# Optimization experiments

Measured on AMD Instinct MI355X. Metric: run time of the kernel, lower is better.

The kernel has to match this reference:

```python
import jax, jax.numpy as jnp
import numpy as np

HEADS = 4
DIM_HEAD = 32
DIM = 128
HIDDEN = HEADS * DIM_HEAD  # 128
EPS = 1e-12  # F.normalize eps


def rms_norm(x, g):
    # F.normalize(x, dim=1) * g * sqrt(C)  with g shape [C]
    n = jnp.sqrt(jnp.sum(x * x, axis=1, keepdims=True))
    return x / jnp.maximum(n, EPS) * g[None, :, None, None] * (x.shape[1] ** 0.5)


def setup_inputs() -> dict:
    key = jax.random.key(0)
    ks = jax.random.split(key, 6)
    x = jax.random.normal(ks[0], (16, DIM, 128, 128), dtype=jnp.float32)
    g1 = jnp.ones((DIM,), dtype=jnp.float32)
    w_qkv = jax.random.normal(ks[1], (3 * HIDDEN, DIM), dtype=jnp.float32) * (1.0 / np.sqrt(DIM))
    w_out = jax.random.normal(ks[2], (DIM, HIDDEN), dtype=jnp.float32) * (1.0 / np.sqrt(HIDDEN))
    b_out = jax.random.normal(ks[3], (DIM,), dtype=jnp.float32) * 0.01
    g2 = jnp.ones((DIM,), dtype=jnp.float32)
    return {"x": x, "g1": g1, "w_qkv": w_qkv, "w_out": w_out, "b_out": b_out, "g2": g2}


def reference(x, g1, w_qkv, w_out, b_out, g2):
    B, C, H, W = x.shape
    n = H * W
    scale = DIM_HEAD ** -0.5
    xn = rms_norm(x, g1)
    # 1x1 conv (no bias) == channel matmul
    qkv = jnp.einsum('oc,bchw->bohw', w_qkv, xn)  # [B, 3*HIDDEN, H, W]
    q, k, v = jnp.split(qkv, 3, axis=1)
    # 'b (h c) x y -> b h c (x y)'
    def to_heads(t):
        return t.reshape(B, HEADS, DIM_HEAD, n)
    q, k, v = to_heads(q), to_heads(k), to_heads(v)
    q = jax.nn.softmax(q, axis=2) * scale   # softmax over head-dim d
    k = jax.nn.softmax(k, axis=3)           # softmax over tokens n
    context = jnp.einsum('bhdn,bhen->bhde', k, v)  # [B,H,d,e] small
    out = jnp.einsum('bhde,bhdn->bhen', context, q)  # [B,H,e,n]
    out = out.reshape(B, HIDDEN, H, W)
    out = jnp.einsum('oc,bchw->bohw', w_out, out) + b_out[None, :, None, None]
    return rms_norm(out, g2)
```

## Files before the change

### kernel.cpp

```cpp
#include <hip/hip_runtime.h>
#include <hip/hip_bf16.h>

#define NTOK 16384
#define SQRT_C 11.313708498984761f
#define QSCALE 0.17677669529663687f

typedef __attribute__((ext_vector_type(8))) short v8s;
typedef __attribute__((ext_vector_type(4))) float v4f;

__device__ inline short f2bf(float f) {
    __hip_bfloat16 h = __float2bfloat16(f);
    return __builtin_bit_cast(short, h);
}
__device__ inline float bf2f(short s) {
    unsigned u = ((unsigned)(unsigned short)s) << 16;
    return __builtin_bit_cast(float, u);
}

__global__ void k0_cvt(const float* __restrict__ wq, short* __restrict__ wbf) {
    int i = blockIdx.x * 256 + threadIdx.x;
    wbf[i] = f2bf(wq[i]);
}

__global__ __launch_bounds__(256, 2) void k1_qkv(
    const float* __restrict__ x, const float* __restrict__ g1,
    const short* __restrict__ wbf, short* __restrict__ qfrag,
    float* __restrict__ pS, float* __restrict__ pC)
{
    __shared__ float xbuf[128][36];
    __shared__ short xn[32][136];
    __shared__ short kvbuf[256][40];
    __shared__ short qbuf[128][33];
    __shared__ float nrm[8][32];
    __shared__ float scl[32];
    __shared__ float g1s[128];

    const int tid = threadIdx.x;
    const int lane = tid & 63;
    const int w = tid >> 6;
    const int qd = lane >> 4;
    const int lm = lane & 15;
    const int b = blockIdx.x >> 5;
    const int chunk = blockIdx.x & 31;
    const size_t xbase = (size_t)b * 128 * NTOK;

    if (tid < 128) g1s[tid] = g1[tid];

    v8s wA[6][4];
    #pragma unroll
    for (int rg = 0; rg < 6; ++rg)
        #pragma unroll
        for (int kk = 0; kk < 4; ++kk)
            wA[rg][kk] = *(const v8s*)(wbf + (96 * w + rg * 16 + lm) * 128 + kk * 32 + qd * 8);

    v4f cacc[2][2];
    #pragma unroll
    for (int i = 0; i < 2; ++i)
        #pragma unroll
        for (int j = 0; j < 2; ++j)
            cacc[i][j] = (v4f){0.f, 0.f, 0.f, 0.f};
    float accS = 0.f;

    for (int st = 0; st < 16; ++st) {
        const int t0 = chunk * 512 + st * 32;
        __syncthreads();
        #pragma unroll
        for (int p = 0; p < 4; ++p) {
            int idx = p * 256 + tid;
            int c = idx >> 3, tq = idx & 7;
            *(float4*)&xbuf[c][tq * 4] =
                *(const float4*)(x + xbase + (size_t)c * NTOK + t0 + tq * 4);
        }
        __syncthreads();
        {
            int t = tid & 31, g = tid >> 5;
            float s = 0.f;
            #pragma unroll
            for (int j = 0; j < 16; ++j) { float v = xbuf[g * 16 + j][t]; s += v * v; }
            nrm[g][t] = s;
        }
        __syncthreads();
        if (tid < 32) {
            float s = 0.f;
            #pragma unroll
            for (int g = 0; g < 8; ++g) s += nrm[g][tid];
            scl[tid] = SQRT_C / fmaxf(sqrtf(s), 1e-12f);
        }
        __syncthreads();
        {
            int t = tid & 31, g = tid >> 5;
            float sc = scl[t];
            #pragma unroll
            for (int j = 0; j < 16; ++j) {
                int c = g * 16 + j;
                xn[t][c] = f2bf(xbuf[c][t] * sc * g1s[c]);
            }
        }
        __syncthreads();
        v4f C[6][2];
        #pragma unroll
        for (int rg = 0; rg < 6; ++rg) {
            C[rg][0] = (v4f){0.f, 0.f, 0.f, 0.f};
            C[rg][1] = (v4f){0.f, 0.f, 0.f, 0.f};
        }
        #pragma unroll
        for (int kk = 0; kk < 4; ++kk) {
            v8s B0 = *(const v8s*)&xn[lm][kk * 32 + qd * 8];
            v8s B1 = *(const v8s*)&xn[16 + lm][kk * 32 + qd * 8];
            #pragma unroll
            for (int rg = 0; rg < 6; ++rg) {
                C[rg][0] = __builtin_amdgcn_mfma_f32_16x16x32_bf16(wA[rg][kk], B0, C[rg][0], 0, 0, 0);
                C[rg][1] = __builtin_amdgcn_mfma_f32_16x16x32_bf16(wA[rg][kk], B1, C[rg][1], 0, 0, 0);
            }
        }
        #pragma unroll
        for (int pr = 0; pr < 3; ++pr) {
            const int R = 96 * w + 32 * pr;
            if (R < 128) {
                #pragma unroll
                for (int tg = 0; tg < 2; ++tg) {
                    float e0[4], e1[4];
                    float m = -1e30f;
                    #pragma unroll
                    for (int r = 0; r < 4; ++r) {
                        e0[r] = C[2 * pr][tg][r];
                        e1[r] = C[2 * pr + 1][tg][r];
                        m = fmaxf(m, fmaxf(e0[r], e1[r]));
                    }
                    m = fmaxf(m, __shfl_xor(m, 16, 64));
                    m = fmaxf(m, __shfl_xor(m, 32, 64));
                    float s = 0.f;
                    #pragma unroll
                    for (int r = 0; r < 4; ++r) {
                        e0[r] = __expf(e0[r] - m);
                        e1[r] = __expf(e1[r] - m);
                        s += e0[r] + e1[r];
                    }
                    s += __shfl_xor(s, 16, 64);
                    s += __shfl_xor(s, 32, 64);
                    float inv = QSCALE / s;
                    int col = tg * 16 + lm;
                    #pragma unroll
                    for (int r = 0; r < 4; ++r) {
                        qbuf[R + qd * 4 + r][col]      = f2bf(e0[r] * inv);
                        qbuf[R + 16 + qd * 4 + r][col] = f2bf(e1[r] * inv);
                    }
                }
            } else {
                #pragma unroll
                for (int f = 0; f < 2; ++f) {
                    const int rg = 2 * pr + f;
                    const int R2 = R + 16 * f;
                    const bool isk = (R2 < 256);
                    #pragma unroll
                    for (int tg = 0; tg < 2; ++tg) {
                        int col = tg * 16 + lm;
                        #pragma unroll
                        for (int r = 0; r < 4; ++r) {
                            float val = C[rg][tg][r];
                            if (isk) val = __expf(val);
                            kvbuf[R2 - 128 + qd * 4 + r][col] = f2bf(val);
                        }
                    }
                }
            }
        }
        __syncthreads();
        if (tid < 128) {
            const short* row = &kvbuf[tid][0];
            float s = 0.f;
            #pragma unroll
            for (int j = 0; j < 32; ++j) s += bf2f(row[j]);
            accS += s;
        }
        {
            const int tb0 = t0 >> 4;
            #pragma unroll
            for (int tbl = 0; tbl < 2; ++tbl) {
                v8s pk;
                #pragma unroll
                for (int j = 0; j < 8; ++j)
                    pk[j] = qbuf[w * 32 + qd * 8 + j][tbl * 16 + lm];
                *(v8s*)(qfrag + ((((size_t)b * 1024 + tb0 + tbl) * 4 + w) << 9) + lane * 8) = pk;
            }
        }
        {
            v8s A0 = *(const v8s*)&kvbuf[w * 32 + lm][qd * 8];
            v8s A1 = *(const v8s*)&kvbuf[w * 32 + 16 + lm][qd * 8];
            v8s B0 = *(const v8s*)&kvbuf[128 + w * 32 + lm][qd * 8];
            v8s B1 = *(const v8s*)&kvbuf[128 + w * 32 + 16 + lm][qd * 8];
            cacc[0][0] = __builtin_amdgcn_mfma_f32_16x16x32_bf16(A0, B0, cacc[0][0], 0, 0, 0);
            cacc[0][1] = __builtin_amdgcn_mfma_f32_16x16x32_bf16(A0, B1, cacc[0][1], 0, 0, 0);
            cacc[1][0] = __builtin_amdgcn_mfma_f32_16x16x32_bf16(A1, B0, cacc[1][0], 0, 0, 0);
            cacc[1][1] = __builtin_amdgcn_mfma_f32_16x16x32_bf16(A1, B1, cacc[1][1], 0, 0, 0);
        }
    }
    if (tid < 128) pS[(size_t)(b * 32 + chunk) * 128 + tid] = accS;
    #pragma unroll
    for (int dg = 0; dg < 2; ++dg)
        #pragma unroll
        for (int eg = 0; eg < 2; ++eg)
            #pragma unroll
            for (int r = 0; r < 4; ++r) {
                int d = dg * 16 + qd * 4 + r;
                int e = eg * 16 + lm;
                pC[(size_t)(b * 32 + chunk) * 4096 + w * 1024 + d * 32 + e] = cacc[dg][eg][r];
            }
}

__global__ void k2_ctx(const float* __restrict__ pS, const float* __restrict__ pC,
                       const float* __restrict__ wout, short* __restrict__ MgT) {
    __shared__ float ctx[32][33];
    __shared__ float Sv[32];
    const int tid = threadIdx.x;
    const int b = blockIdx.x >> 2, h = blockIdx.x & 3;
    if (tid < 32) {
        float s = 0.f;
        for (int ch = 0; ch < 32; ++ch) s += pS[(size_t)(b * 32 + ch) * 128 + h * 32 + tid];
        Sv[tid] = s;
    }
    __syncthreads();
    #pragma unroll
    for (int k = 0; k < 4; ++k) {
        int de = tid + k * 256;
        float s = 0.f;
        for (int ch = 0; ch < 32; ++ch) s += pC[(size_t)(b * 32 + ch) * 4096 + h * 1024 + de];
        ctx[de >> 5][de & 31] = s / Sv[de >> 5];
    }
    __syncthreads();
    #pragma unroll
    for (int k = 0; k < 16; ++k) {
        int idx = tid + k * 256;
        int d = idx & 31, o = idx >> 5;
        float m = 0.f;
        #pragma unroll
        for (int e = 0; e < 32; ++e) m += wout[o * 128 + h * 32 + e] * ctx[d][e];
        MgT[((size_t)b * 128 + o) * 128 + h * 32 + d] = f2bf(m);
    }
}

__global__ __launch_bounds__(256) void k3_out(
    const short* __restrict__ qfrag, const short* __restrict__ MgT,
    const float* __restrict__ bo, const float* __restrict__ g2,
    float* __restrict__ out)
{
    __shared__ float part[4][128];
    __shared__ float scl[128];
    const int tid = threadIdx.x;
    const int lane = tid & 63, w = tid >> 6;
    const int qd = lane >> 4, lm = lane & 15;
    const int b = blockIdx.x >> 7;
    const int t0 = (blockIdx.x & 127) << 7;
    const int tb0 = t0 >> 4;

    v8s A[2][4];
    #pragma unroll
    for (int rg = 0; rg < 2; ++rg)
        #pragma unroll
        for (int kk = 0; kk < 4; ++kk)
            A[rg][kk] = *(const v8s*)(MgT + ((size_t)b * 128 + 32 * w + rg * 16 + lm) * 128 + kk * 32 + qd * 8);

    v4f C[2][8];
    #pragma unroll
    for (int rg = 0; rg < 2; ++rg)
        #pragma unroll
        for (int tb = 0; tb < 8; ++tb)
            C[rg][tb] = (v4f){0.f, 0.f, 0.f, 0.f};

    #pragma unroll
    for (int tb = 0; tb < 8; ++tb)
        #pragma unroll
        for (int kk = 0; kk < 4; ++kk) {
            v8s B = *(const v8s*)(qfrag + ((((size_t)b * 1024 + tb0 + tb) * 4 + kk) << 9) + lane * 8);
            C[0][tb] = __builtin_amdgcn_mfma_f32_16x16x32_bf16(A[0][kk], B, C[0][tb], 0, 0, 0);
            C[1][tb] = __builtin_amdgcn_mfma_f32_16x16x32_bf16(A[1][kk], B, C[1][tb], 0, 0, 0);
        }

    float bov[2][4], g2v[2][4];
    #pragma unroll
    for (int rg = 0; rg < 2; ++rg)
        #pragma unroll
        for (int r = 0; r < 4; ++r) {
            int o = 32 * w + rg * 16 + qd * 4 + r;
            bov[rg][r] = bo[o];
            g2v[rg][r] = g2[o];
        }
    #pragma unroll
    for (int tb = 0; tb < 8; ++tb) {
        float ss = 0.f;
        #pragma unroll
        for (int rg = 0; rg < 2; ++rg)
            #pragma unroll
            for (int r = 0; r < 4; ++r) {
                C[rg][tb][r] += bov[rg][r];
                ss += C[rg][tb][r] * C[rg][tb][r];
            }
        ss += __shfl_xor(ss, 16, 64);
        ss += __shfl_xor(ss, 32, 64);
        if (lane < 16) part[w][tb * 16 + lane] = ss;
    }
    __syncthreads();
    if (tid < 128) {
        float s = part[0][tid] + part[1][tid] + part[2][tid] + part[3][tid];
        scl[tid] = SQRT_C / fmaxf(sqrtf(s), 1e-12f);
    }
    __syncthreads();
    #pragma unroll
    for (int tb = 0; tb < 8; ++tb) {
        float sc = scl[tb * 16 + lm];
        #pragma unroll
        for (int rg = 0; rg < 2; ++rg)
            #pragma unroll
            for (int r = 0; r < 4; ++r) {
                int o = 32 * w + rg * 16 + qd * 4 + r;
                out[((size_t)b * 128 + o) * NTOK + t0 + tb * 16 + lm] = C[rg][tb][r] * sc * g2v[rg][r];
            }
    }
}

extern "C" void kernel_launch(void* const* d_in, const int* in_sizes, int n_in,
                              void* d_out, int out_size, void* d_ws, size_t ws_size,
                              hipStream_t stream) {
    const float* x    = (const float*)d_in[0];
    const float* g1   = (const float*)d_in[1];
    const float* wqkv = (const float*)d_in[2];
    const float* wout = (const float*)d_in[3];
    const float* bo   = (const float*)d_in[4];
    const float* g2   = (const float*)d_in[5];
    float* out = (float*)d_out;
    char* ws = (char*)d_ws;
    short* qfrag = (short*)ws;
    float* pS = (float*)(ws + 67108864);
    float* pC = (float*)(ws + 67371008);
    short* MgT = (short*)(ws + 75759616);
    short* wbf = (short*)(ws + 76283904);

    k0_cvt<<<192, 256, 0, stream>>>(wqkv, wbf);
    k1_qkv<<<512, 256, 0, stream>>>(x, g1, wbf, qfrag, pS, pC);
    k2_ctx<<<64, 256, 0, stream>>>(pS, pC, wout, MgT);
    k3_out<<<2048, 256, 0, stream>>>(qfrag, MgT, bo, g2, out);
}
```

Measured before the change: 334.6 us.

## Prefetch x into registers, defer RMS scale past QKV matmul, cut barriers

The QKV kernel now loads the next x tile into registers while the current one is processed, and stops staging x through shared memory. The RMS-norm scale is applied to the MFMA output instead of the input, and g1 is folded into the bf16 weights. Together this drops five block barriers per step to two, using an LDS-only waitcnt barrier. Q is written transposed so its fragment stores become vector reads. K row sums are built from shuffle reductions instead of a serial LDS scan. The cost is extra registers for the prefetch, and rounding changes because the unnormalized x is cast to bf16 before scaling.

```diff
diff --git a/kernel.cpp b/kernel.cpp
--- a/kernel.cpp
+++ b/kernel.cpp
@@ -6,6 +6,7 @@
 #define QSCALE 0.17677669529663687f
 
 typedef __attribute__((ext_vector_type(8))) short v8s;
+typedef __attribute__((ext_vector_type(4))) short v4s;
 typedef __attribute__((ext_vector_type(4))) float v4f;
 
 __device__ inline short f2bf(float f) {
@@ -16,24 +17,27 @@
     unsigned u = ((unsigned)(unsigned short)s) << 16;
     return __builtin_bit_cast(float, u);
 }
-
-__global__ void k0_cvt(const float* __restrict__ wq, short* __restrict__ wbf) {
+__device__ inline void lds_barrier() {
+    __builtin_amdgcn_sched_barrier(0);
+    asm volatile("s_waitcnt lgkmcnt(0)" ::: "memory");
+    __builtin_amdgcn_s_barrier();
+    __builtin_amdgcn_sched_barrier(0);
+}
+
+__global__ void k0_cvt(const float* __restrict__ wq, const float* __restrict__ g1,
+                       short* __restrict__ wbf) {
     int i = blockIdx.x * 256 + threadIdx.x;
-    wbf[i] = f2bf(wq[i]);
+    wbf[i] = f2bf(wq[i] * g1[i & 127]);
 }
 
 __global__ __launch_bounds__(256, 2) void k1_qkv(
-    const float* __restrict__ x, const float* __restrict__ g1,
-    const short* __restrict__ wbf, short* __restrict__ qfrag,
-    float* __restrict__ pS, float* __restrict__ pC)
+    const float* __restrict__ x, const short* __restrict__ wbf,
+    short* __restrict__ qfrag, float* __restrict__ pS, float* __restrict__ pC)
 {
-    __shared__ float xbuf[128][36];
-    __shared__ short xn[32][136];
-    __shared__ short kvbuf[256][40];
-    __shared__ short qbuf[128][33];
-    __shared__ float nrm[8][32];
-    __shared__ float scl[32];
-    __shared__ float g1s[128];
+    __shared__ __align__(16) short xn[32][136];
+    __shared__ __align__(16) short kvbuf[256][40];
+    __shared__ __align__(16) short qbufT[32][136];
+    __shared__ __align__(16) float nrm[4][32];
 
     const int tid = threadIdx.x;
     const int lane = tid & 63;
@@ -43,8 +47,8 @@
     const int b = blockIdx.x >> 5;
     const int chunk = blockIdx.x & 31;
     const size_t xbase = (size_t)b * 128 * NTOK;
-
-    if (tid < 128) g1s[tid] = g1[tid];
+    const int crow = tid >> 3;
+    const int tq4 = (tid & 7) * 4;
 
     v8s wA[6][4];
     #pragma unroll
@@ -59,44 +63,42 @@
         #pragma unroll
         for (int j = 0; j < 2; ++j)
             cacc[i][j] = (v4f){0.f, 0.f, 0.f, 0.f};
-    float accS = 0.f;
+    float accSr[6][4] = {};
+
+    v4f xv[4];
+    auto loadx = [&](int tt) {
+        #pragma unroll
+        for (int p = 0; p < 4; ++p)
+            xv[p] = *(const v4f*)(x + xbase + (size_t)(p * 32 + crow) * NTOK + tt + tq4);
+    };
+    loadx(chunk * 512);
 
     for (int st = 0; st < 16; ++st) {
         const int t0 = chunk * 512 + st * 32;
-        __syncthreads();
-        #pragma unroll
-        for (int p = 0; p < 4; ++p) {
-            int idx = p * 256 + tid;
-            int c = idx >> 3, tq = idx & 7;
-            *(float4*)&xbuf[c][tq * 4] =
-                *(const float4*)(x + xbase + (size_t)c * NTOK + t0 + tq * 4);
-        }
-        __syncthreads();
-        {
-            int t = tid & 31, g = tid >> 5;
-            float s = 0.f;
-            #pragma unroll
-            for (int j = 0; j < 16; ++j) { float v = xbuf[g * 16 + j][t]; s += v * v; }
-            nrm[g][t] = s;
-        }
-        __syncthreads();
-        if (tid < 32) {
-            float s = 0.f;
-            #pragma unroll
-            for (int g = 0; g < 8; ++g) s += nrm[g][tid];
-            scl[tid] = SQRT_C / fmaxf(sqrtf(s), 1e-12f);
-        }
-        __syncthreads();
-        {
-            int t = tid & 31, g = tid >> 5;
-            float sc = scl[t];
-            #pragma unroll
-            for (int j = 0; j < 16; ++j) {
-                int c = g * 16 + j;
-                xn[t][c] = f2bf(xbuf[c][t] * sc * g1s[c]);
-            }
-        }
-        __syncthreads();
+
+        float s[4];
+        #pragma unroll
+        for (int j = 0; j < 4; ++j) {
+            float acc = 0.f;
+            #pragma unroll
+            for (int p = 0; p < 4; ++p) { float v = xv[p][j]; acc += v * v; }
+            s[j] = acc;
+        }
+        #pragma unroll
+        for (int j = 0; j < 4; ++j) {
+            s[j] += __shfl_xor(s[j], 8, 64);
+            s[j] += __shfl_xor(s[j], 16, 64);
+            s[j] += __shfl_xor(s[j], 32, 64);
+        }
+        if (lane < 8) *(v4f*)&nrm[w][lane * 4] = (v4f){s[0], s[1], s[2], s[3]};
+        #pragma unroll
+        for (int p = 0; p < 4; ++p)
+            #pragma unroll
+            for (int j = 0; j < 4; ++j)
+                xn[tq4 + j][p * 32 + crow] = f2bf(xv[p][j]);
+        loadx(st < 15 ? t0 + 32 : chunk * 512);
+        lds_barrier();
+
         v4f C[6][2];
         #pragma unroll
         for (int rg = 0; rg < 6; ++rg) {
@@ -113,38 +115,47 @@
                 C[rg][1] = __builtin_amdgcn_mfma_f32_16x16x32_bf16(wA[rg][kk], B1, C[rg][1], 0, 0, 0);
             }
         }
+        float sA = nrm[0][lm] + nrm[1][lm] + nrm[2][lm] + nrm[3][lm];
+        float sB = nrm[0][16 + lm] + nrm[1][16 + lm] + nrm[2][16 + lm] + nrm[3][16 + lm];
+        float scl0 = SQRT_C / fmaxf(sqrtf(sA), 1e-12f);
+        float scl1 = SQRT_C / fmaxf(sqrtf(sB), 1e-12f);
+
         #pragma unroll
         for (int pr = 0; pr < 3; ++pr) {
             const int R = 96 * w + 32 * pr;
             if (R < 128) {
                 #pragma unroll
                 for (int tg = 0; tg < 2; ++tg) {
+                    const float sclt = tg ? scl1 : scl0;
                     float e0[4], e1[4];
                     float m = -1e30f;
                     #pragma unroll
                     for (int r = 0; r < 4; ++r) {
-                        e0[r] = C[2 * pr][tg][r];
-                        e1[r] = C[2 * pr + 1][tg][r];
+                        e0[r] = C[2 * pr][tg][r] * sclt;
+                        e1[r] = C[2 * pr + 1][tg][r] * sclt;
                         m = fmaxf(m, fmaxf(e0[r], e1[r]));
                     }
                     m = fmaxf(m, __shfl_xor(m, 16, 64));
                     m = fmaxf(m, __shfl_xor(m, 32, 64));
-                    float s = 0.f;
+                    float ssum = 0.f;
                     #pragma unroll
                     for (int r = 0; r < 4; ++r) {
                         e0[r] = __expf(e0[r] - m);
                         e1[r] = __expf(e1[r] - m);
-                        s += e0[r] + e1[r];
-                    }
-                    s += __shfl_xor(s, 16, 64);
-                    s += __shfl_xor(s, 32, 64);
-                    float inv = QSCALE / s;
-                    int col = tg * 16 + lm;
+                        ssum += e0[r] + e1[r];
+                    }
+                    ssum += __shfl_xor(ssum, 16, 64);
+                    ssum += __shfl_xor(ssum, 32, 64);
+                    const float inv = QSCALE / ssum;
+                    const int t = tg * 16 + lm;
+                    v4s p0, p1;
                     #pragma unroll
                     for (int r = 0; r < 4; ++r) {
-                        qbuf[R + qd * 4 + r][col]      = f2bf(e0[r] * inv);
-                        qbuf[R + 16 + qd * 4 + r][col] = f2bf(e1[r] * inv);
-                    }
+                        p0[r] = f2bf(e0[r] * inv);
+                        p1[r] = f2bf(e1[r] * inv);
+                    }
+                    *(v4s*)&qbufT[t][R + qd * 4] = p0;
+                    *(v4s*)&qbufT[t][R + 16 + qd * 4] = p1;
                 }
             } else {
                 #pragma unroll
@@ -152,39 +163,43 @@
                     const int rg = 2 * pr + f;
                     const int R2 = R + 16 * f;
                     const bool isk = (R2 < 256);
+                    float part[4] = {0.f, 0.f, 0.f, 0.f};
                     #pragma unroll
                     for (int tg = 0; tg < 2; ++tg) {
-                        int col = tg * 16 + lm;
+                        const float sclt = tg ? scl1 : scl0;
+                        const int col = tg * 16 + lm;
                         #pragma unroll
                         for (int r = 0; r < 4; ++r) {
-                            float val = C[rg][tg][r];
+                            float val = C[rg][tg][r] * sclt;
                             if (isk) val = __expf(val);
-                            kvbuf[R2 - 128 + qd * 4 + r][col] = f2bf(val);
+                            short vb = f2bf(val);
+                            kvbuf[R2 - 128 + qd * 4 + r][col] = vb;
+                            if (isk) part[r] += bf2f(vb);
                         }
                     }
+                    if (isk) {
+                        #pragma unroll
+                        for (int r = 0; r < 4; ++r) {
+                            float p = part[r];
+                            p += __shfl_xor(p, 1, 64);
+                            p += __shfl_xor(p, 2, 64);
+                            p += __shfl_xor(p, 4, 64);
+                            p += __shfl_xor(p, 8, 64);
+                            accSr[rg][r] += p;
+                        }
+                    }
                 }
             }
         }
-        __syncthreads();
-        if (tid < 128) {
-            const short* row = &kvbuf[tid][0];
-            float s = 0.f;
-            #pragma unroll
-            for (int j = 0; j < 32; ++j) s += bf2f(row[j]);
-            accS += s;
-        }
+        lds_barrier();
+
         {
-            const int tb0 = t0 >> 4;
+            const int tb0 = chunk * 32 + st * 2;
             #pragma unroll
             for (int tbl = 0; tbl < 2; ++tbl) {
-                v8s pk;
-                #pragma unroll
-                for (int j = 0; j < 8; ++j)
-                    pk[j] = qbuf[w * 32 + qd * 8 + j][tbl * 16 + lm];
+                v8s pk = *(const v8s*)&qbufT[tbl * 16 + lm][w * 32 + qd * 8];
                 *(v8s*)(qfrag + ((((size_t)b * 1024 + tb0 + tbl) * 4 + w) << 9) + lane * 8) = pk;
             }
-        }
-        {
             v8s A0 = *(const v8s*)&kvbuf[w * 32 + lm][qd * 8];
             v8s A1 = *(const v8s*)&kvbuf[w * 32 + 16 + lm][qd * 8];
             v8s B0 = *(const v8s*)&kvbuf[128 + w * 32 + lm][qd * 8];
@@ -195,7 +210,18 @@
             cacc[1][1] = __builtin_amdgcn_mfma_f32_16x16x32_bf16(A1, B1, cacc[1][1], 0, 0, 0);
         }
     }
-    if (tid < 128) pS[(size_t)(b * 32 + chunk) * 128 + tid] = accS;
+
+    if ((w == 1 || w == 2) && lm == 0) {
+        #pragma unroll
+        for (int rg = 0; rg < 6; ++rg) {
+            const int R = 96 * w + 16 * rg;
+            if (R >= 128 && R < 256) {
+                #pragma unroll
+                for (int r = 0; r < 4; ++r)
+                    pS[(size_t)(b * 32 + chunk) * 128 + (R - 128) + qd * 4 + r] = accSr[rg][r];
+            }
+        }
+    }
     #pragma unroll
     for (int dg = 0; dg < 2; ++dg)
         #pragma unroll
@@ -335,8 +361,8 @@
     short* MgT = (short*)(ws + 75759616);
     short* wbf = (short*)(ws + 76283904);
 
-    k0_cvt<<<192, 256, 0, stream>>>(wqkv, wbf);
-    k1_qkv<<<512, 256, 0, stream>>>(x, g1, wbf, qfrag, pS, pC);
+    k0_cvt<<<192, 256, 0, stream>>>(wqkv, g1, wbf);
+    k1_qkv<<<512, 256, 0, stream>>>(x, wbf, qfrag, pS, pC);
     k2_ctx<<<64, 256, 0, stream>>>(pS, pC, wout, MgT);
     k3_out<<<2048, 256, 0, stream>>>(qfrag, MgT, bo, g2, out);
 }
```

After: 333.2 us. Within noise of the previous version (-0.4%).
